# Kernel optimization log

Hardware: AMD Instinct MI355X
Metric: run time of the kernel (lower is better)

The kernel has to match this reference:

```python
import jax, jax.numpy as jnp
import numpy as np

B, D_IN, D_OUT = 16384, 2048, 2048
BN_EPS = 1e-5


def setup_inputs() -> dict:
    key = jax.random.key(0)
    ks = jax.random.split(key, 6)
    return {
        "x": jax.random.normal(ks[0], (B, D_IN), dtype=jnp.float32),
        "base_weight": jax.random.normal(ks[1], (D_OUT, D_IN), dtype=jnp.float32) * 0.1,
        "bias": jnp.zeros((D_OUT,), dtype=jnp.float32),
        "center": jax.random.normal(ks[2], (D_IN,), dtype=jnp.float32),
        "sharpness": jnp.ones((D_IN,), dtype=jnp.float32),
        "gamma": jnp.ones((D_OUT,), dtype=jnp.float32),
        "beta": jnp.zeros((D_OUT,), dtype=jnp.float32),
        "top_k": 256,
    }


def reference(x, base_weight, bias, center, sharpness, gamma, beta, top_k):
    # fuzzy membership: sigmoid(sharpness * (x - center))  -> [B, D_in]
    mu = jax.nn.sigmoid(sharpness * (x - center))
    b, d = mu.shape

    # OWA weighted membership: keep top_k memberships, scaled by
    # normalized linspace(1.0, 0.1, top_k) weights; zeros elsewhere.
    order = jnp.argsort(-mu, axis=1)                       # descending sort indices
    sorted_vals = jnp.take_along_axis(mu, order, axis=1)
    w = jnp.linspace(1.0, 0.1, top_k, dtype=mu.dtype)
    w = w / w.sum()
    owa = jnp.zeros_like(mu).at[
        jnp.arange(b)[:, None], order[:, :top_k]
    ].set(w[None, :] * sorted_vals[:, :top_k])

    # per-sample scaled matmul: bmm(W * mu_exp, x) == (owa * x) @ W^T
    out = (owa * x) @ base_weight.T + bias                 # [B, D_out]
    out = jax.nn.relu(out)

    # BatchNorm1d in training mode: batch mean, biased variance
    mean = out.mean(axis=0)
    var = out.var(axis=0)
    y = (out - mean) * jax.lax.rsqrt(var + BN_EPS) * gamma + beta
    return (y, mu)
```

## Files before the change

kernel.cpp:

```cpp
#include <hip/hip_runtime.h>
#include <stdint.h>

#define NB 16384
#define DI 2048
#define DO 2048
#define KTOP 256
#define LIST_CAP 384
#define MT (NB / 256)

typedef __attribute__((ext_vector_type(4))) float f32x4;
typedef __attribute__((ext_vector_type(8))) short s16x8;
typedef __attribute__((ext_vector_type(8))) unsigned short u16x8;

#define OWA_C0 7.10227273e-3f
#define OWA_C1 2.50668449e-5f

__device__ __forceinline__ ushort f2bf(float f) {
  uint32_t u = __float_as_uint(f);
  uint32_t r = (u + 0x7FFFu + ((u >> 16) & 1u)) >> 16;
  return (ushort)r;
}

__device__ __forceinline__ void gld_lds16(const void* g, void* l) {
  __builtin_amdgcn_global_load_lds((__attribute__((address_space(1))) void*)g,
                                   (__attribute__((address_space(3))) void*)l,
                                   16, 0, 0);
}

__global__ __launch_bounds__(256) void k_cvt(const float* __restrict__ W,
                                             ushort* __restrict__ Wb) {
  size_t i = ((size_t)blockIdx.x * 256 + threadIdx.x) * 8;
  float4 a = *(const float4*)(W + i);
  float4 b = *(const float4*)(W + i + 4);
  u16x8 o;
  o[0] = f2bf(a.x); o[1] = f2bf(a.y); o[2] = f2bf(a.z); o[3] = f2bf(a.w);
  o[4] = f2bf(b.x); o[5] = f2bf(b.y); o[6] = f2bf(b.z); o[7] = f2bf(b.w);
  *(u16x8*)(Wb + i) = o;
}

__global__ __launch_bounds__(256) void k_topk(
    const float* __restrict__ x, const float* __restrict__ center,
    const float* __restrict__ sharp, float* __restrict__ mu_out,
    ushort* __restrict__ A) {
  __shared__ __align__(16) float w_lds[DI];
  __shared__ uint32_t histR[8 * 256];
  __shared__ uint64_t list[LIST_CAP];
  __shared__ uint32_t scal[8];

  const int t = threadIdx.x;
  const int lane = t & 63;
  const int wv = t >> 6;
  const int row = blockIdx.x;
  const int base = t * 8;

  const float* xr = x + (size_t)row * DI + base;
  float4 xa = *(const float4*)(xr);
  float4 xb = *(const float4*)(xr + 4);
  float4 ca = *(const float4*)(center + base);
  float4 cb = *(const float4*)(center + base + 4);
  float4 sa = *(const float4*)(sharp + base);
  float4 sb = *(const float4*)(sharp + base + 4);

  float xv[8] = {xa.x, xa.y, xa.z, xa.w, xb.x, xb.y, xb.z, xb.w};
  float cv[8] = {ca.x, ca.y, ca.z, ca.w, cb.x, cb.y, cb.z, cb.w};
  float sv[8] = {sa.x, sa.y, sa.z, sa.w, sb.x, sb.y, sb.z, sb.w};
  float muv[8];
  uint32_t bits[8];
#pragma unroll
  for (int e = 0; e < 8; ++e) {
    float s = sv[e] * (xv[e] - cv[e]);
    float m = 1.0f / (1.0f + __expf(-s));
    muv[e] = m;
    bits[e] = __float_as_uint(m);
  }
  if (mu_out) {
    float4 m0; m0.x = muv[0]; m0.y = muv[1]; m0.z = muv[2]; m0.w = muv[3];
    float4 m1; m1.x = muv[4]; m1.y = muv[5]; m1.z = muv[6]; m1.w = muv[7];
    *(float4*)(mu_out + (size_t)row * DI + base) = m0;
    *(float4*)(mu_out + (size_t)row * DI + base + 4) = m1;
  }
  float4 z4; z4.x = z4.y = z4.z = z4.w = 0.f;
  *(float4*)(w_lds + base) = z4;
  *(float4*)(w_lds + base + 4) = z4;
  if (t == 0) scal[2] = 0;

  const uint32_t rep = (uint32_t)(t & 7) * 256u;

  uint32_t nhi = 0;
#pragma unroll
  for (int e = 0; e < 8; ++e) nhi += (bits[e] >> 24) == 0x3Fu;
#pragma unroll
  for (int off = 1; off < 64; off <<= 1) nhi += __shfl_xor(nhi, off);
  if (lane == 0) scal[4 + wv] = nhi;
  __syncthreads();
  const uint32_t c_hi = scal[4] + scal[5] + scal[6] + scal[7];

  uint32_t maskHi = 0xFF000000u, pfx = 0x3F000000u, krem = KTOP;
  if (c_hi < KTOP) {
#pragma unroll
    for (int i = 0; i < 8; ++i) histR[t + 256 * i] = 0;
    __syncthreads();
#pragma unroll
    for (int e = 0; e < 8; ++e) atomicAdd(&histR[rep + (bits[e] >> 24)], 1u);
    __syncthreads();
    if (wv == 0) {
      uint32_t c0 = 0, c1 = 0, c2 = 0, c3 = 0;
#pragma unroll
      for (int r = 0; r < 8; ++r) {
        const uint32_t* h = &histR[r * 256 + lane * 4];
        c0 += h[0]; c1 += h[1]; c2 += h[2]; c3 += h[3];
      }
      uint32_t s3 = c3, s2 = c2 + s3, s1 = c1 + s2, s0 = c0 + s1;
      uint32_t Tl = s0, suf = s0;
#pragma unroll
      for (int off = 1; off < 64; off <<= 1) {
        uint32_t v = __shfl_down(suf, off);
        if (lane + off < 64) suf += v;
      }
      uint32_t above = suf - Tl;
      uint32_t SS[4] = {s0 + above, s1 + above, s2 + above, s3 + above};
      uint32_t cc[4] = {c0, c1, c2, c3};
#pragma unroll
      for (int j = 0; j < 4; ++j) {
        if (SS[j] >= KTOP && (SS[j] - cc[j]) < KTOP) {
          scal[0] = (uint32_t)(lane * 4 + j);
          scal[1] = SS[j] - cc[j];
        }
      }
    }
    __syncthreads();
    pfx = scal[0] << 24;
    krem = KTOP - scal[1];
  }

#pragma unroll
  for (int i = 0; i < 8; ++i) histR[t + 256 * i] = 0;
  __syncthreads();
#pragma unroll
  for (int e = 0; e < 8; ++e) {
    if ((bits[e] & maskHi) == pfx)
      atomicAdd(&histR[rep + ((bits[e] >> 16) & 255u)], 1u);
  }
  __syncthreads();
  if (wv == 0) {
    uint32_t c0 = 0, c1 = 0, c2 = 0, c3 = 0;
#pragma unroll
    for (int r = 0; r < 8; ++r) {
      const uint32_t* h = &histR[r * 256 + lane * 4];
      c0 += h[0]; c1 += h[1]; c2 += h[2]; c3 += h[3];
    }
    uint32_t s3 = c3, s2 = c2 + s3, s1 = c1 + s2, s0 = c0 + s1;
    uint32_t Tl = s0, suf = s0;
#pragma unroll
    for (int off = 1; off < 64; off <<= 1) {
      uint32_t v = __shfl_down(suf, off);
      if (lane + off < 64) suf += v;
    }
    uint32_t above = suf - Tl;
    uint32_t SS[4] = {s0 + above, s1 + above, s2 + above, s3 + above};
    uint32_t cc[4] = {c0, c1, c2, c3};
#pragma unroll
    for (int j = 0; j < 4; ++j) {
      if (SS[j] >= krem && (SS[j] - cc[j]) < krem) {
        scal[0] = (uint32_t)(lane * 4 + j);
        scal[1] = SS[j] - cc[j];
      }
    }
  }
  __syncthreads();
  const uint32_t tb = pfx | (scal[0] << 16);

  const uint64_t lmask_lt = (1ull << lane) - 1ull;
#pragma unroll
  for (int e = 0; e < 8; ++e) {
    bool pr = (bits[e] >= tb);
    uint64_t m = __ballot(pr);
    uint32_t cnt = (uint32_t)__popcll(m);
    if (cnt) {
      uint32_t wbase = 0;
      if (lane == 0) wbase = atomicAdd(&scal[2], cnt);
      wbase = __shfl(wbase, 0);
      if (pr) {
        uint32_t pos = wbase + (uint32_t)__popcll(m & lmask_lt);
        if (pos < LIST_CAP)
          list[pos] = ((uint64_t)bits[e] << 32) |
                      (uint64_t)(uint32_t)(DI - 1 - (base + e));
      }
    }
  }
  __syncthreads();
  int L = (int)scal[2];
  if (L > LIST_CAP) L = LIST_CAP;

  for (int sIdx = t; sIdx < L; sIdx += 256) {
    uint64_t key = list[sIdx];
    int rank = 0;
#pragma unroll 4
    for (int j = 0; j < L; ++j) rank += (int)(list[j] > key);
    if (rank < KTOP) {
      int idx = DI - 1 - (int)((uint32_t)key & 0xFFFFFFFFu);
      w_lds[idx] = OWA_C0 - OWA_C1 * (float)rank;
    }
  }
  __syncthreads();

  u16x8 ov;
#pragma unroll
  for (int e = 0; e < 8; ++e) ov[e] = f2bf(w_lds[base + e] * muv[e] * xv[e]);
  *(u16x8*)(A + (size_t)row * DI + base) = ov;
}

#define HALFS 8192

#define MFMA(a, b, c) __builtin_amdgcn_mfma_f32_16x16x32_bf16(a, b, c, 0, 0, 0)

#define STAGE_A(U, h)                                                       \
  do {                                                                      \
    ushort* sl = lA + (((((U) & 1) << 1) + (h)) * HALFS);                   \
    gld_lds16(pA0 + (size_t)((h) * 128) * DI + (size_t)(U) * 64, sl + d0);  \
    gld_lds16(pA0 + (size_t)((h) * 128 + 64) * DI + (size_t)(U) * 64,       \
              sl + d1);                                                     \
  } while (0)

#define STAGE_B(U, h)                                                       \
  do {                                                                      \
    ushort* sl = lB + (((((U) & 1) << 1) + (h)) * HALFS);                   \
    gld_lds16(pB0 + (size_t)((h) * 128) * DI + (size_t)(U) * 64, sl + d0);  \
    gld_lds16(pB0 + (size_t)((h) * 128 + 64) * DI + (size_t)(U) * 64,       \
              sl + d1);                                                     \
  } while (0)

#define RD_A(BUF, slotp, rowb)                                              \
  do {                                                                      \
    const ushort* rp_ = (slotp) + ((rowb) + fr) * 64;                       \
    BUF[0] = *(const s16x8*)(rp_ + c0);                                     \
    BUF[1] = *(const s16x8*)(rp_ + c1);                                     \
    BUF[2] = *(const s16x8*)(rp_ + 16 * 64 + c0);                           \
    BUF[3] = *(const s16x8*)(rp_ + 16 * 64 + c1);                           \
  } while (0)

#define RD_B(slotp)                                                         \
  do {                                                                      \
    _Pragma("unroll") for (int ni = 0; ni < 4; ++ni) {                      \
      breg[ni][0] = *(const s16x8*)((slotp) + ni * 1024 + boff + c0);       \
      breg[ni][1] = *(const s16x8*)((slotp) + ni * 1024 + boff + c1);       \
    }                                                                       \
  } while (0)

#define MFMA_PHASE(q, BUF)                                                  \
  do {                                                                      \
    __builtin_amdgcn_s_setprio(1);                                          \
    _Pragma("unroll") for (int ni = 0; ni < 4; ++ni) {                      \
      acc[2 * (q)][ni] = MFMA(BUF[0], breg[ni][0], acc[2 * (q)][ni]);       \
      acc[2 * (q)][ni] = MFMA(BUF[1], breg[ni][1], acc[2 * (q)][ni]);       \
      acc[2 * (q) + 1][ni] = MFMA(BUF[2], breg[ni][0], acc[2 * (q) + 1][ni]); \
      acc[2 * (q) + 1][ni] = MFMA(BUF[3], breg[ni][1], acc[2 * (q) + 1][ni]); \
    }                                                                       \
    __builtin_amdgcn_s_setprio(0);                                          \
  } while (0)

#define PHASE(q, RD_STMT, STAGE_STMT, BUF, POST_STMT, TAIL_STMT, LG)        \
  do {                                                                      \
    RD_STMT;                                                                \
    STAGE_STMT;                                                             \
    __builtin_amdgcn_s_barrier();                                           \
    asm volatile("s_waitcnt lgkmcnt(" LG ")" ::: "memory");                 \
    __builtin_amdgcn_sched_barrier(0);                                      \
    MFMA_PHASE(q, BUF);                                                     \
    POST_STMT;                                                              \
    TAIL_STMT;                                                              \
    __builtin_amdgcn_s_barrier();                                           \
  } while (0)

__global__ __launch_bounds__(512, 2) void k_gemm(
    const ushort* __restrict__ A, const ushort* __restrict__ Wb,
    const float* __restrict__ bias, float* __restrict__ outp,
    float* __restrict__ psum, float* __restrict__ psumsq) {
  __shared__ __align__(16) ushort lA[4 * HALFS];
  __shared__ __align__(16) ushort lB[4 * HALFS];

  const int t = threadIdx.x;
  const int lane = t & 63;
  const int wv = t >> 6;
  const int wm = wv >> 2;
  const int wn = wv & 3;
  const int wm32 = wm * 32;
  const int fr = lane & 15;
  const int kg = lane >> 4;
  const int s = fr & 7;

  int bid = blockIdx.x;
  int orig = (bid & 7) * 64 + (bid >> 3);
  const int nb = orig & 7;
  const int mb = orig >> 3;
  const int m0 = mb * 256;
  const int n0 = nb * 256;

  const int srow0 = t >> 3;
  const int scol = ((t & 7) ^ (srow0 & 7)) * 8;
  const ushort* pA0 = A + (size_t)(m0 + srow0) * DI + scol;
  const ushort* pB0 = Wb + (size_t)(n0 + srow0) * DI + scol;
  const int d0 = t * 8;
  const int d1 = (512 + t) * 8;

  f32x4 acc[8][4];
#pragma unroll
  for (int i = 0; i < 8; ++i)
#pragma unroll
    for (int j = 0; j < 4; ++j) acc[i][j] = (f32x4){0.f, 0.f, 0.f, 0.f};

  const int c0 = (kg ^ s) * 8;
  const int c1 = ((4 + kg) ^ s) * 8;
  const int boff = ((wn & 1) * 64 + fr) * 64;

  s16x8 breg[4][2];
  s16x8 bufA_[4], bufB_[4];

  STAGE_B(0, 0); STAGE_B(0, 1);
  STAGE_A(0, 0); STAGE_A(0, 1);
  STAGE_B(1, 0); STAGE_B(1, 1);
  asm volatile("s_waitcnt vmcnt(6)" ::: "memory");
  __builtin_amdgcn_s_barrier();
  RD_B(lB + (wn >> 1) * HALFS);
  RD_A(bufA_, lA, wm32);

#pragma unroll 1
  for (int T = 0; T < 31; ++T) {
    const ushort* lAcur = lA + ((T & 1) << 1) * HALFS;
    const ushort* lAnxt = lA + (((T + 1) & 1) << 1) * HALFS;
    const ushort* sBnxt = lB + ((((T + 1) & 1) << 1) + (wn >> 1)) * HALFS;

    PHASE(0, RD_A(bufB_, lAcur, 64 + wm32), STAGE_A(T + 1, 0), bufA_, ,
          asm volatile("s_waitcnt vmcnt(6)" ::: "memory"), "4");
    PHASE(1, RD_A(bufA_, lAcur + HALFS, wm32), STAGE_A(T + 1, 1), bufB_, , ,
          "4");
    PHASE(2, RD_A(bufB_, lAcur + HALFS, 64 + wm32),
          if (T < 30) STAGE_B(T + 2, 0), bufA_, ,
          if (T < 30) { asm volatile("s_waitcnt vmcnt(4)" ::: "memory"); }
          else { asm volatile("s_waitcnt vmcnt(2)" ::: "memory"); }, "4");
    PHASE(3, RD_A(bufA_, lAnxt, wm32), if (T < 30) STAGE_B(T + 2, 1), bufB_,
          RD_B(sBnxt), , "4");
  }
  {
    const ushort* lAcur = lA + 2 * HALFS;
    PHASE(0, RD_A(bufB_, lAcur, 64 + wm32), , bufA_, ,
          asm volatile("s_waitcnt vmcnt(0)" ::: "memory"), "4");
    PHASE(1, RD_A(bufA_, lAcur + HALFS, wm32), , bufB_, , , "4");
    PHASE(2, RD_A(bufB_, lAcur + HALFS, 64 + wm32), , bufA_, , , "4");
    PHASE(3, , , bufB_, , , "0");
  }

  __syncthreads();
  float* colsum = (float*)lA;
  float* colsq = colsum + 256;
  if (t < 256) { colsum[t] = 0.f; colsq[t] = 0.f; }
  __syncthreads();
#pragma unroll
  for (int ni = 0; ni < 4; ++ni) {
    const int n = n0 + wn * 64 + ni * 16 + fr;
    const float bv = bias[n];
    float cs = 0.f, cq = 0.f;
#pragma unroll
    for (int mi = 0; mi < 8; ++mi) {
      const int rowb = m0 + 64 * (mi >> 1) + wm32 + 16 * (mi & 1) + kg * 4;
      f32x4 v = acc[mi][ni];
#pragma unroll
      for (int r = 0; r < 4; ++r) {
        float zz = fmaxf(v[r] + bv, 0.f);
        outp[(size_t)(rowb + r) * DO + n] = zz;
        cs += zz;
        cq += zz * zz;
      }
    }
    cs += __shfl_xor(cs, 16); cq += __shfl_xor(cq, 16);
    cs += __shfl_xor(cs, 32); cq += __shfl_xor(cq, 32);
    if (kg == 0) {
      atomicAdd(&colsum[wn * 64 + ni * 16 + fr], cs);
      atomicAdd(&colsq[wn * 64 + ni * 16 + fr], cq);
    }
  }
  __syncthreads();
  if (t < 256) {
    psum[(size_t)mb * DO + n0 + t] = colsum[t];
    psumsq[(size_t)mb * DO + n0 + t] = colsq[t];
  }
}

__global__ __launch_bounds__(256) void k_bnfin(
    const float* __restrict__ psum, const float* __restrict__ psumsq,
    const float* __restrict__ gamma, const float* __restrict__ beta,
    float* __restrict__ scaleA, float* __restrict__ shiftA) {
  int n = blockIdx.x * 256 + threadIdx.x;
  float s = 0.f, q = 0.f;
  for (int r = 0; r < MT; ++r) {
    s += psum[(size_t)r * DO + n];
    q += psumsq[(size_t)r * DO + n];
  }
  float mean = s * (1.0f / (float)NB);
  float var = q * (1.0f / (float)NB) - mean * mean;
  var = fmaxf(var, 0.f);
  float rstd = rsqrtf(var + 1e-5f);
  float sc = gamma[n] * rstd;
  scaleA[n] = sc;
  shiftA[n] = beta[n] - mean * sc;
}

__global__ __launch_bounds__(256) void k_bnapply(float* __restrict__ outp,
                                                 const float* __restrict__ scaleA,
                                                 const float* __restrict__ shiftA) {
  size_t i = ((size_t)blockIdx.x * 256 + threadIdx.x) * 4;
  int n = (int)(i & (DO - 1));
  float4 v = *(float4*)(outp + i);
  float4 sc = *(const float4*)(scaleA + n);
  float4 sh = *(const float4*)(shiftA + n);
  v.x = v.x * sc.x + sh.x;
  v.y = v.y * sc.y + sh.y;
  v.z = v.z * sc.z + sh.z;
  v.w = v.w * sc.w + sh.w;
  *(float4*)(outp + i) = v;
}

__global__ __launch_bounds__(256) void k_mu(const float* __restrict__ x,
                                            const float* __restrict__ center,
                                            const float* __restrict__ sharp,
                                            float* __restrict__ mu_out) {
  const int t = threadIdx.x;
  const int row = blockIdx.x;
  const int base = t * 8;
  const float* xr = x + (size_t)row * DI + base;
  float4 xa = *(const float4*)(xr);
  float4 xb = *(const float4*)(xr + 4);
  float4 ca = *(const float4*)(center + base);
  float4 cb = *(const float4*)(center + base + 4);
  float4 sa = *(const float4*)(sharp + base);
  float4 sb = *(const float4*)(sharp + base + 4);
  float xv[8] = {xa.x, xa.y, xa.z, xa.w, xb.x, xb.y, xb.z, xb.w};
  float cv[8] = {ca.x, ca.y, ca.z, ca.w, cb.x, cb.y, cb.z, cb.w};
  float sv[8] = {sa.x, sa.y, sa.z, sa.w, sb.x, sb.y, sb.z, sb.w};
  float mu[8];
#pragma unroll
  for (int e = 0; e < 8; ++e) {
    float s = sv[e] * (xv[e] - cv[e]);
    mu[e] = 1.0f / (1.0f + __expf(-s));
  }
  float4 m0; m0.x = mu[0]; m0.y = mu[1]; m0.z = mu[2]; m0.w = mu[3];
  float4 m1; m1.x = mu[4]; m1.y = mu[5]; m1.z = mu[6]; m1.w = mu[7];
  *(float4*)(mu_out + (size_t)row * DI + base) = m0;
  *(float4*)(mu_out + (size_t)row * DI + base + 4) = m1;
}

extern "C" void kernel_launch(void* const* d_in, const int* in_sizes, int n_in,
                              void* d_out, int out_size, void* d_ws, size_t ws_size,
                              hipStream_t stream) {
  (void)in_sizes; (void)n_in; (void)out_size;
  const float* x = (const float*)d_in[0];
  const float* W = (const float*)d_in[1];
  const float* bias = (const float*)d_in[2];
  const float* center = (const float*)d_in[3];
  const float* sharp = (const float*)d_in[4];
  const float* gamma = (const float*)d_in[5];
  const float* beta = (const float*)d_in[6];

  float* outY = (float*)d_out;
  float* outMu = outY + (size_t)NB * DO;

  const size_t A_BYTES = (size_t)NB * DI * 2;
  const size_t WB_BYTES = (size_t)DO * DI * 2;
  const size_t PS_BYTES = (size_t)MT * DO * 4;
  const size_t SC_BYTES = (size_t)DO * 4;
  const size_t NEED_BIG = A_BYTES + WB_BYTES + 2 * PS_BYTES + 2 * SC_BYTES;

  char* p = (char*)d_ws;
  bool bigws = (ws_size >= NEED_BIG);
  ushort* A;
  if (bigws) { A = (ushort*)p; p += A_BYTES; }
  else       { A = (ushort*)outMu; }
  ushort* Wb = (ushort*)p; p += WB_BYTES;
  float* psum = (float*)p; p += PS_BYTES;
  float* psumsq = (float*)p; p += PS_BYTES;
  float* scaleA = (float*)p; p += SC_BYTES;
  float* shiftA = (float*)p;

  k_cvt<<<dim3((DO * DI) / (256 * 8)), dim3(256), 0, stream>>>(W, Wb);
  k_topk<<<dim3(NB), dim3(256), 0, stream>>>(x, center, sharp,
                                             bigws ? outMu : (float*)nullptr, A);
  k_gemm<<<dim3((NB / 256) * (DO / 256)), dim3(512), 0, stream>>>(A, Wb, bias, outY,
                                                                  psum, psumsq);
  k_bnfin<<<dim3(DO / 256), dim3(256), 0, stream>>>(psum, psumsq, gamma, beta,
                                                    scaleA, shiftA);
  k_bnapply<<<dim3((size_t)NB * DO / 4 / 256), dim3(256), 0, stream>>>(outY, scaleA,
                                                                       shiftA);
  if (!bigws) k_mu<<<dim3(NB), dim3(256), 0, stream>>>(x, center, sharp, outMu);
}
```

Baseline: 371.5 us.

## Bucket top-k candidates by radix digit to shrink per-element rank comparisons

Rewrites the final ranking step of the top-k selection. Candidates are placed into list segments grouped by their second radix byte, using prefix offsets saved from the histogram. Each element is then ranked only against candidates in its own bucket instead of scanning the whole candidate list. The aim is to cut the O(L^2) LDS comparison loop in the top-k kernel, at the cost of two small LDS arrays and per-element atomics.

```diff
diff --git a/kernel.cpp b/kernel.cpp
--- a/kernel.cpp
+++ b/kernel.cpp
@@ -45,6 +45,8 @@
   __shared__ __align__(16) float w_lds[DI];
   __shared__ uint32_t histR[8 * 256];
   __shared__ uint64_t list[LIST_CAP];
+  __shared__ uint32_t babove[256];
+  __shared__ uint32_t bcnt[256];
   __shared__ uint32_t scal[8];
 
   const int t = threadIdx.x;
@@ -82,7 +84,7 @@
   float4 z4; z4.x = z4.y = z4.z = z4.w = 0.f;
   *(float4*)(w_lds + base) = z4;
   *(float4*)(w_lds + base + 4) = z4;
-  if (t == 0) scal[2] = 0;
+  if (t == 0) scal[3] = 0;
 
   const uint32_t rep = (uint32_t)(t & 7) * 256u;
 
@@ -95,7 +97,7 @@
   __syncthreads();
   const uint32_t c_hi = scal[4] + scal[5] + scal[6] + scal[7];
 
-  uint32_t maskHi = 0xFF000000u, pfx = 0x3F000000u, krem = KTOP;
+  uint32_t pfx = 0x3F000000u, krem = KTOP;
   if (c_hi < KTOP) {
 #pragma unroll
     for (int i = 0; i < 8; ++i) histR[t + 256 * i] = 0;
@@ -132,13 +134,15 @@
     pfx = scal[0] << 24;
     krem = KTOP - scal[1];
   }
+  const uint32_t pfxbyte = pfx >> 24;
+  const uint32_t nsuper = KTOP - krem;
 
 #pragma unroll
   for (int i = 0; i < 8; ++i) histR[t + 256 * i] = 0;
   __syncthreads();
 #pragma unroll
   for (int e = 0; e < 8; ++e) {
-    if ((bits[e] & maskHi) == pfx)
+    if ((bits[e] >> 24) == pfxbyte)
       atomicAdd(&histR[rep + ((bits[e] >> 16) & 255u)], 1u);
   }
   __syncthreads();
@@ -159,47 +163,58 @@
     uint32_t above = suf - Tl;
     uint32_t SS[4] = {s0 + above, s1 + above, s2 + above, s3 + above};
     uint32_t cc[4] = {c0, c1, c2, c3};
+    uint4 ba, bc;
+    ba.x = SS[0] - cc[0]; ba.y = SS[1] - cc[1];
+    ba.z = SS[2] - cc[2]; ba.w = SS[3] - cc[3];
+    bc.x = cc[0]; bc.y = cc[1]; bc.z = cc[2]; bc.w = cc[3];
+    *(uint4*)&babove[lane * 4] = ba;
+    *(uint4*)&bcnt[lane * 4] = bc;
 #pragma unroll
     for (int j = 0; j < 4; ++j) {
       if (SS[j] >= krem && (SS[j] - cc[j]) < krem) {
         scal[0] = (uint32_t)(lane * 4 + j);
-        scal[1] = SS[j] - cc[j];
       }
     }
   }
   __syncthreads();
   const uint32_t tb = pfx | (scal[0] << 16);
 
-  const uint64_t lmask_lt = (1ull << lane) - 1ull;
+  histR[t] = 0;
+  __syncthreads();
+
+  int lo8[8], hi8[8];
 #pragma unroll
   for (int e = 0; e < 8; ++e) {
-    bool pr = (bits[e] >= tb);
-    uint64_t m = __ballot(pr);
-    uint32_t cnt = (uint32_t)__popcll(m);
-    if (cnt) {
-      uint32_t wbase = 0;
-      if (lane == 0) wbase = atomicAdd(&scal[2], cnt);
-      wbase = __shfl(wbase, 0);
-      if (pr) {
-        uint32_t pos = wbase + (uint32_t)__popcll(m & lmask_lt);
-        if (pos < LIST_CAP)
-          list[pos] = ((uint64_t)bits[e] << 32) |
-                      (uint64_t)(uint32_t)(DI - 1 - (base + e));
+    lo8[e] = 0; hi8[e] = 0;
+    if (bits[e] >= tb) {
+      uint64_t key = ((uint64_t)bits[e] << 32) |
+                     (uint64_t)(uint32_t)(DI - 1 - (base + e));
+      uint32_t lo, hi, slot;
+      if ((bits[e] >> 24) == pfxbyte) {
+        uint32_t d = (bits[e] >> 16) & 255u;
+        uint32_t idx = atomicAdd(&histR[d], 1u);
+        lo = nsuper + babove[d];
+        hi = lo + bcnt[d];
+        slot = lo + idx;
+      } else {
+        uint32_t idx = atomicAdd(&scal[3], 1u);
+        lo = 0; hi = nsuper; slot = idx;
       }
-    }
-  }
-  __syncthreads();
-  int L = (int)scal[2];
-  if (L > LIST_CAP) L = LIST_CAP;
-
-  for (int sIdx = t; sIdx < L; sIdx += 256) {
-    uint64_t key = list[sIdx];
-    int rank = 0;
-#pragma unroll 4
-    for (int j = 0; j < L; ++j) rank += (int)(list[j] > key);
-    if (rank < KTOP) {
-      int idx = DI - 1 - (int)((uint32_t)key & 0xFFFFFFFFu);
-      w_lds[idx] = OWA_C0 - OWA_C1 * (float)rank;
+      if (slot < LIST_CAP) list[slot] = key;
+      lo8[e] = (int)lo;
+      hi8[e] = (int)(hi > LIST_CAP ? LIST_CAP : hi);
+    }
+  }
+  __syncthreads();
+
+#pragma unroll
+  for (int e = 0; e < 8; ++e) {
+    if (bits[e] >= tb) {
+      uint64_t key = ((uint64_t)bits[e] << 32) |
+                     (uint64_t)(uint32_t)(DI - 1 - (base + e));
+      int r = lo8[e];
+      for (int j = lo8[e]; j < hi8[e]; ++j) r += (int)(list[j] > key);
+      if (r < KTOP) w_lds[base + e] = OWA_C0 - OWA_C1 * (float)r;
     }
   }
   __syncthreads();
```

After: 331.0 us. 1.12x faster.
